# Kernel optimization log

Measured on AMD Instinct MI355X. Metric: run time of the kernel, lower is better.

## Reference

```python
import jax, jax.numpy as jnp
import numpy as np

B, N = 2048, 8192
K = 64          # subset size / number of relaxation steps
TAU = 1.0
EPS = 1e-10


def setup_inputs() -> dict:
    key = jax.random.key(0)
    k1, k2 = jax.random.split(key)
    scores = jax.random.normal(k1, (B, N), dtype=jnp.float32)
    # Gumbel(0,1) noise, same as torch.distributions.Gumbel(zeros, ones).sample()
    u = jax.random.uniform(k2, (B, N), dtype=jnp.float32, minval=1e-20, maxval=1.0)
    g = -jnp.log(-jnp.log(u))
    return {"scores": scores, "g": g}


def reference(scores, g):
    # Perturb scores with Gumbel noise
    s0 = scores + g  # [B, N]
    khot0 = jnp.zeros_like(s0)
    onehot0 = jnp.zeros_like(s0)

    def step(carry, _):
        s, khot, onehot_approx = carry
        khot_mask = jnp.maximum(1.0 - onehot_approx, EPS)   # suppress picked items
        s = s + jnp.log(khot_mask)
        onehot_approx = jax.nn.softmax(s / TAU, axis=1)
        return (s, khot + onehot_approx, onehot_approx), None

    (_, khot, _), _ = jax.lax.scan(step, (s0, khot0, onehot0), None, length=K)
    # hard=False -> return relaxed k-hot vector
    return khot
```

## Files before the change

kernel.cpp:

```cpp
#include <hip/hip_runtime.h>
#include <math.h>


#define BROWS 2048
#define NCOLS 8192
#define KSTEPS 64

#define THREADS 256
#define EPT (NCOLS / THREADS)

__global__ __launch_bounds__(THREADS, 4) void gumbel_subset_kernel(
    const float* __restrict__ scores,
    const float* __restrict__ g,
    float* __restrict__ out)
{
    const int row = blockIdx.x;
    const int t = threadIdx.x;
    const float* __restrict__ srow = scores + (size_t)row * NCOLS;
    const float* __restrict__ grow = g + (size_t)row * NCOLS;
    float* __restrict__ orow = out + (size_t)row * NCOLS;

    float v[EPT];
    float kh[EPT];

    float m = -INFINITY;
#pragma unroll
    for (int c = 0; c < EPT / 4; ++c) {
        const int idx = c * (THREADS * 4) + t * 4;
        const float4 a = *reinterpret_cast<const float4*>(srow + idx);
        const float4 b = *reinterpret_cast<const float4*>(grow + idx);
        const float s0 = a.x + b.x;
        const float s1 = a.y + b.y;
        const float s2 = a.z + b.z;
        const float s3 = a.w + b.w;
        v[c * 4 + 0] = s0;
        v[c * 4 + 1] = s1;
        v[c * 4 + 2] = s2;
        v[c * 4 + 3] = s3;
        m = fmaxf(m, fmaxf(fmaxf(s0, s1), fmaxf(s2, s3)));
    }

    __shared__ float red[2][8];
    const int wave = t >> 6;
    const int lane = t & 63;

#pragma unroll
    for (int off = 32; off > 0; off >>= 1)
        m = fmaxf(m, __shfl_xor(m, off, 64));
    if (lane == 0) red[0][wave] = m;
    __syncthreads();
    m = fmaxf(fmaxf(red[0][0], red[0][1]), fmaxf(red[0][2], red[0][3]));
    __syncthreads();

#pragma unroll
    for (int e = 0; e < EPT; ++e) {
        v[e] = __expf(v[e] - m);
        kh[e] = 0.0f;
    }

#pragma unroll 2
    for (int it = 0; it < KSTEPS; ++it) {
        float s = 0.0f;
#pragma unroll
        for (int e = 0; e < EPT; ++e) s += v[e];
#pragma unroll
        for (int off = 32; off > 0; off >>= 1)
            s += __shfl_xor(s, off, 64);

        const int buf = it & 1;
        if (lane == 0) red[buf][wave] = s;
        __syncthreads();
        const float S = (red[buf][0] + red[buf][1]) + (red[buf][2] + red[buf][3]);
        const float rinv = __builtin_amdgcn_rcpf(S);

#pragma unroll
        for (int e = 0; e < EPT; ++e) {
            const float w = v[e] * rinv;
            kh[e] += w;
            v[e] = __builtin_fmaf(-w, v[e], v[e]);
        }
    }

#pragma unroll
    for (int c = 0; c < EPT / 4; ++c) {
        const int idx = c * (THREADS * 4) + t * 4;
        float4 o;
        o.x = kh[c * 4 + 0];
        o.y = kh[c * 4 + 1];
        o.z = kh[c * 4 + 2];
        o.w = kh[c * 4 + 3];
        *reinterpret_cast<float4*>(orow + idx) = o;
    }
}

extern "C" void kernel_launch(void* const* d_in, const int* in_sizes, int n_in,
                              void* d_out, int out_size, void* d_ws, size_t ws_size,
                              hipStream_t stream) {
    const float* scores = (const float*)d_in[0];
    const float* g = (const float*)d_in[1];
    float* out = (float*)d_out;
    (void)in_sizes; (void)n_in; (void)out_size; (void)d_ws; (void)ws_size;

    gumbel_subset_kernel<<<BROWS, THREADS, 0, stream>>>(scores, g, out);
}
```

Before: 110.6 us.

## Double threads per row and fuse row-sum into the update loop

```diff
diff --git a/kernel.cpp b/kernel.cpp
--- a/kernel.cpp
+++ b/kernel.cpp
@@ -6,10 +6,11 @@
 #define NCOLS 8192
 #define KSTEPS 64
 
-#define THREADS 256
+#define THREADS 512
 #define EPT (NCOLS / THREADS)
+#define NWAVE (THREADS / 64)
 
-__global__ __launch_bounds__(THREADS, 4) void gumbel_subset_kernel(
+__global__ __launch_bounds__(THREADS, 8) void gumbel_subset_kernel(
     const float* __restrict__ scores,
     const float* __restrict__ g,
     float* __restrict__ out)
@@ -40,7 +41,7 @@
         m = fmaxf(m, fmaxf(fmaxf(s0, s1), fmaxf(s2, s3)));
     }
 
-    __shared__ float red[2][8];
+    __shared__ float red[2][NWAVE];
     const int wave = t >> 6;
     const int lane = t & 63;
 
@@ -49,20 +50,24 @@
         m = fmaxf(m, __shfl_xor(m, off, 64));
     if (lane == 0) red[0][wave] = m;
     __syncthreads();
-    m = fmaxf(fmaxf(red[0][0], red[0][1]), fmaxf(red[0][2], red[0][3]));
+    m = fmaxf(fmaxf(fmaxf(red[0][0], red[0][1]), fmaxf(red[0][2], red[0][3])),
+              fmaxf(fmaxf(red[0][4], red[0][5]), fmaxf(red[0][6], red[0][7])));
     __syncthreads();
 
+    float sa = 0.0f, sb = 0.0f, sc = 0.0f, sd = 0.0f;
 #pragma unroll
-    for (int e = 0; e < EPT; ++e) {
-        v[e] = __expf(v[e] - m);
-        kh[e] = 0.0f;
+    for (int e = 0; e < EPT; e += 4) {
+        v[e + 0] = __expf(v[e + 0] - m);
+        v[e + 1] = __expf(v[e + 1] - m);
+        v[e + 2] = __expf(v[e + 2] - m);
+        v[e + 3] = __expf(v[e + 3] - m);
+        kh[e + 0] = 0.0f; kh[e + 1] = 0.0f; kh[e + 2] = 0.0f; kh[e + 3] = 0.0f;
+        sa += v[e + 0]; sb += v[e + 1]; sc += v[e + 2]; sd += v[e + 3];
     }
 
 #pragma unroll 2
     for (int it = 0; it < KSTEPS; ++it) {
-        float s = 0.0f;
-#pragma unroll
-        for (int e = 0; e < EPT; ++e) s += v[e];
+        float s = (sa + sb) + (sc + sd);
 #pragma unroll
         for (int off = 32; off > 0; off >>= 1)
             s += __shfl_xor(s, off, 64);
@@ -70,14 +75,23 @@
         const int buf = it & 1;
         if (lane == 0) red[buf][wave] = s;
         __syncthreads();
-        const float S = (red[buf][0] + red[buf][1]) + (red[buf][2] + red[buf][3]);
+        const float S = ((red[buf][0] + red[buf][1]) + (red[buf][2] + red[buf][3])) +
+                        ((red[buf][4] + red[buf][5]) + (red[buf][6] + red[buf][7]));
         const float rinv = __builtin_amdgcn_rcpf(S);
 
+        sa = 0.0f; sb = 0.0f; sc = 0.0f; sd = 0.0f;
 #pragma unroll
-        for (int e = 0; e < EPT; ++e) {
-            const float w = v[e] * rinv;
-            kh[e] += w;
-            v[e] = __builtin_fmaf(-w, v[e], v[e]);
+        for (int e = 0; e < EPT; e += 4) {
+            const float w0 = v[e + 0] * rinv;
+            const float w1 = v[e + 1] * rinv;
+            const float w2 = v[e + 2] * rinv;
+            const float w3 = v[e + 3] * rinv;
+            kh[e + 0] += w0; kh[e + 1] += w1; kh[e + 2] += w2; kh[e + 3] += w3;
+            v[e + 0] = __builtin_fmaf(-w0, v[e + 0], v[e + 0]);
+            v[e + 1] = __builtin_fmaf(-w1, v[e + 1], v[e + 1]);
+            v[e + 2] = __builtin_fmaf(-w2, v[e + 2], v[e + 2]);
+            v[e + 3] = __builtin_fmaf(-w3, v[e + 3], v[e + 3]);
+            sa += v[e + 0]; sb += v[e + 1]; sc += v[e + 2]; sd += v[e + 3];
         }
     }
 
```

Result: slower. 130.4 us (+17.9%).

## Store softmax state in packed fp16 and fuse row-sum into the update pass

Applied to the files above, without the earlier changes.

```diff
diff --git a/kernel.cpp b/kernel.cpp
--- a/kernel.cpp
+++ b/kernel.cpp
@@ -1,6 +1,8 @@
 #include <hip/hip_runtime.h>
 #include <math.h>
 
+
+typedef _Float16 h2 __attribute__((ext_vector_type(2)));
 
 #define BROWS 2048
 #define NCOLS 8192
@@ -8,6 +10,8 @@
 
 #define THREADS 256
 #define EPT (NCOLS / THREADS)
+#define NPAIR (EPT / 2)
+#define NWAVE (THREADS / 64)
 
 __global__ __launch_bounds__(THREADS, 4) void gumbel_subset_kernel(
     const float* __restrict__ scores,
@@ -20,27 +24,22 @@
     const float* __restrict__ grow = g + (size_t)row * NCOLS;
     float* __restrict__ orow = out + (size_t)row * NCOLS;
 
-    float v[EPT];
-    float kh[EPT];
-
+    float s0[EPT];
     float m = -INFINITY;
 #pragma unroll
     for (int c = 0; c < EPT / 4; ++c) {
         const int idx = c * (THREADS * 4) + t * 4;
         const float4 a = *reinterpret_cast<const float4*>(srow + idx);
         const float4 b = *reinterpret_cast<const float4*>(grow + idx);
-        const float s0 = a.x + b.x;
-        const float s1 = a.y + b.y;
-        const float s2 = a.z + b.z;
-        const float s3 = a.w + b.w;
-        v[c * 4 + 0] = s0;
-        v[c * 4 + 1] = s1;
-        v[c * 4 + 2] = s2;
-        v[c * 4 + 3] = s3;
-        m = fmaxf(m, fmaxf(fmaxf(s0, s1), fmaxf(s2, s3)));
+        s0[c * 4 + 0] = a.x + b.x;
+        s0[c * 4 + 1] = a.y + b.y;
+        s0[c * 4 + 2] = a.z + b.z;
+        s0[c * 4 + 3] = a.w + b.w;
+        m = fmaxf(m, fmaxf(fmaxf(s0[c * 4 + 0], s0[c * 4 + 1]),
+                           fmaxf(s0[c * 4 + 2], s0[c * 4 + 3])));
     }
 
-    __shared__ float red[2][8];
+    __shared__ float red[2][NWAVE];
     const int wave = t >> 6;
     const int lane = t & 63;
 
@@ -52,17 +51,21 @@
     m = fmaxf(fmaxf(red[0][0], red[0][1]), fmaxf(red[0][2], red[0][3]));
     __syncthreads();
 
+    h2 v[NPAIR];
+    h2 kh[NPAIR];
+    float part = 0.0f;
 #pragma unroll
-    for (int e = 0; e < EPT; ++e) {
-        v[e] = __expf(v[e] - m);
-        kh[e] = 0.0f;
+    for (int p = 0; p < NPAIR; ++p) {
+        const float e0 = __expf(s0[2 * p + 0] - m);
+        const float e1 = __expf(s0[2 * p + 1] - m);
+        v[p] = (h2){(_Float16)e0, (_Float16)e1};
+        kh[p] = (h2){(_Float16)0.0f, (_Float16)0.0f};
+        part += e0 + e1;
     }
 
 #pragma unroll 2
     for (int it = 0; it < KSTEPS; ++it) {
-        float s = 0.0f;
-#pragma unroll
-        for (int e = 0; e < EPT; ++e) s += v[e];
+        float s = part;
 #pragma unroll
         for (int off = 32; off > 0; off >>= 1)
             s += __shfl_xor(s, off, 64);
@@ -71,24 +74,39 @@
         if (lane == 0) red[buf][wave] = s;
         __syncthreads();
         const float S = (red[buf][0] + red[buf][1]) + (red[buf][2] + red[buf][3]);
-        const float rinv = __builtin_amdgcn_rcpf(S);
+        const float rinvf = __builtin_amdgcn_rcpf(S);
+        const _Float16 rh = (_Float16)rinvf;
+        const h2 rinv2 = (h2){rh, rh};
 
+        h2 a0 = (h2){(_Float16)0.0f, (_Float16)0.0f};
+        h2 a1 = a0, a2 = a0, a3 = a0;
 #pragma unroll
-        for (int e = 0; e < EPT; ++e) {
-            const float w = v[e] * rinv;
-            kh[e] += w;
-            v[e] = __builtin_fmaf(-w, v[e], v[e]);
+        for (int p = 0; p < NPAIR; p += 4) {
+            const h2 w0 = v[p + 0] * rinv2;
+            const h2 w1 = v[p + 1] * rinv2;
+            const h2 w2 = v[p + 2] * rinv2;
+            const h2 w3 = v[p + 3] * rinv2;
+            kh[p + 0] += w0; kh[p + 1] += w1; kh[p + 2] += w2; kh[p + 3] += w3;
+            v[p + 0] = __builtin_elementwise_fma(-w0, v[p + 0], v[p + 0]);
+            v[p + 1] = __builtin_elementwise_fma(-w1, v[p + 1], v[p + 1]);
+            v[p + 2] = __builtin_elementwise_fma(-w2, v[p + 2], v[p + 2]);
+            v[p + 3] = __builtin_elementwise_fma(-w3, v[p + 3], v[p + 3]);
+            a0 += v[p + 0]; a1 += v[p + 1]; a2 += v[p + 2]; a3 += v[p + 3];
         }
+        const h2 a01 = a0 + a1;
+        const h2 a23 = a2 + a3;
+        const h2 aa = a01 + a23;
+        part = (float)aa.x + (float)aa.y;
     }
 
 #pragma unroll
     for (int c = 0; c < EPT / 4; ++c) {
         const int idx = c * (THREADS * 4) + t * 4;
         float4 o;
-        o.x = kh[c * 4 + 0];
-        o.y = kh[c * 4 + 1];
-        o.z = kh[c * 4 + 2];
-        o.w = kh[c * 4 + 3];
+        o.x = (float)kh[2 * c + 0].x;
+        o.y = (float)kh[2 * c + 0].y;
+        o.z = (float)kh[2 * c + 1].x;
+        o.w = (float)kh[2 * c + 1].y;
         *reinterpret_cast<float4*>(orow + idx) = o;
     }
 }
```

New measurement: 103.8 us. 6.1% less time.

## Pack softmax state in fp16 pairs, process two rows per block, fuse sum

Applied to the files above, without the earlier changes.

```diff
diff --git a/kernel.cpp b/kernel.cpp
--- a/kernel.cpp
+++ b/kernel.cpp
@@ -1,95 +1,141 @@
 #include <hip/hip_runtime.h>
 #include <math.h>
 
+
+typedef _Float16 h2 __attribute__((ext_vector_type(2)));
 
 #define BROWS 2048
 #define NCOLS 8192
 #define KSTEPS 64
 
 #define THREADS 256
+#define RPB 2
 #define EPT (NCOLS / THREADS)
+#define NPAIR (EPT / 2)
+#define NWAVE (THREADS / 64)
 
-__global__ __launch_bounds__(THREADS, 4) void gumbel_subset_kernel(
+__global__ __launch_bounds__(THREADS, 2) void gumbel_subset_kernel(
     const float* __restrict__ scores,
     const float* __restrict__ g,
     float* __restrict__ out)
 {
-    const int row = blockIdx.x;
     const int t = threadIdx.x;
-    const float* __restrict__ srow = scores + (size_t)row * NCOLS;
-    const float* __restrict__ grow = g + (size_t)row * NCOLS;
-    float* __restrict__ orow = out + (size_t)row * NCOLS;
+    const size_t baseA = (size_t)(blockIdx.x * RPB) * NCOLS;
+    const size_t baseB = baseA + NCOLS;
 
-    float v[EPT];
-    float kh[EPT];
-
-    float m = -INFINITY;
+    float sA[EPT], sB[EPT];
+    float mA = -INFINITY, mB = -INFINITY;
 #pragma unroll
     for (int c = 0; c < EPT / 4; ++c) {
         const int idx = c * (THREADS * 4) + t * 4;
-        const float4 a = *reinterpret_cast<const float4*>(srow + idx);
-        const float4 b = *reinterpret_cast<const float4*>(grow + idx);
-        const float s0 = a.x + b.x;
-        const float s1 = a.y + b.y;
-        const float s2 = a.z + b.z;
-        const float s3 = a.w + b.w;
-        v[c * 4 + 0] = s0;
-        v[c * 4 + 1] = s1;
-        v[c * 4 + 2] = s2;
-        v[c * 4 + 3] = s3;
-        m = fmaxf(m, fmaxf(fmaxf(s0, s1), fmaxf(s2, s3)));
+        const float4 a0 = *reinterpret_cast<const float4*>(scores + baseA + idx);
+        const float4 g0 = *reinterpret_cast<const float4*>(g + baseA + idx);
+        sA[c * 4 + 0] = a0.x + g0.x;
+        sA[c * 4 + 1] = a0.y + g0.y;
+        sA[c * 4 + 2] = a0.z + g0.z;
+        sA[c * 4 + 3] = a0.w + g0.w;
+        mA = fmaxf(mA, fmaxf(fmaxf(sA[c * 4 + 0], sA[c * 4 + 1]),
+                             fmaxf(sA[c * 4 + 2], sA[c * 4 + 3])));
+        const float4 a1 = *reinterpret_cast<const float4*>(scores + baseB + idx);
+        const float4 g1 = *reinterpret_cast<const float4*>(g + baseB + idx);
+        sB[c * 4 + 0] = a1.x + g1.x;
+        sB[c * 4 + 1] = a1.y + g1.y;
+        sB[c * 4 + 2] = a1.z + g1.z;
+        sB[c * 4 + 3] = a1.w + g1.w;
+        mB = fmaxf(mB, fmaxf(fmaxf(sB[c * 4 + 0], sB[c * 4 + 1]),
+                             fmaxf(sB[c * 4 + 2], sB[c * 4 + 3])));
     }
 
-    __shared__ float red[2][8];
+    __shared__ float red[2][2 * NWAVE];
     const int wave = t >> 6;
     const int lane = t & 63;
 
 #pragma unroll
-    for (int off = 32; off > 0; off >>= 1)
-        m = fmaxf(m, __shfl_xor(m, off, 64));
-    if (lane == 0) red[0][wave] = m;
+    for (int off = 32; off > 0; off >>= 1) {
+        mA = fmaxf(mA, __shfl_xor(mA, off, 64));
+        mB = fmaxf(mB, __shfl_xor(mB, off, 64));
+    }
+    if (lane == 0) { red[0][wave] = mA; red[0][NWAVE + wave] = mB; }
     __syncthreads();
-    m = fmaxf(fmaxf(red[0][0], red[0][1]), fmaxf(red[0][2], red[0][3]));
+    mA = fmaxf(fmaxf(red[0][0], red[0][1]), fmaxf(red[0][2], red[0][3]));
+    mB = fmaxf(fmaxf(red[0][4], red[0][5]), fmaxf(red[0][6], red[0][7]));
     __syncthreads();
 
+    h2 vA[NPAIR], khA[NPAIR], vB[NPAIR], khB[NPAIR];
+    float partA = 0.0f, partB = 0.0f;
 #pragma unroll
-    for (int e = 0; e < EPT; ++e) {
-        v[e] = __expf(v[e] - m);
-        kh[e] = 0.0f;
+    for (int p = 0; p < NPAIR; ++p) {
+        const float eA0 = __expf(sA[2 * p + 0] - mA);
+        const float eA1 = __expf(sA[2 * p + 1] - mA);
+        vA[p] = (h2){(_Float16)eA0, (_Float16)eA1};
+        khA[p] = (h2){(_Float16)0.0f, (_Float16)0.0f};
+        partA += eA0 + eA1;
+        const float eB0 = __expf(sB[2 * p + 0] - mB);
+        const float eB1 = __expf(sB[2 * p + 1] - mB);
+        vB[p] = (h2){(_Float16)eB0, (_Float16)eB1};
+        khB[p] = (h2){(_Float16)0.0f, (_Float16)0.0f};
+        partB += eB0 + eB1;
     }
 
 #pragma unroll 2
     for (int it = 0; it < KSTEPS; ++it) {
-        float s = 0.0f;
+        float sa = partA, sb = partB;
 #pragma unroll
-        for (int e = 0; e < EPT; ++e) s += v[e];
-#pragma unroll
-        for (int off = 32; off > 0; off >>= 1)
-            s += __shfl_xor(s, off, 64);
+        for (int off = 32; off > 0; off >>= 1) {
+            sa += __shfl_xor(sa, off, 64);
+            sb += __shfl_xor(sb, off, 64);
+        }
 
         const int buf = it & 1;
-        if (lane == 0) red[buf][wave] = s;
+        if (lane == 0) { red[buf][wave] = sa; red[buf][NWAVE + wave] = sb; }
         __syncthreads();
-        const float S = (red[buf][0] + red[buf][1]) + (red[buf][2] + red[buf][3]);
-        const float rinv = __builtin_amdgcn_rcpf(S);
+        const float SA = (red[buf][0] + red[buf][1]) + (red[buf][2] + red[buf][3]);
+        const float SB = (red[buf][4] + red[buf][5]) + (red[buf][6] + red[buf][7]);
+        const float rAf = __builtin_amdgcn_rcpf(SA);
+        const float rBf = __builtin_amdgcn_rcpf(SB);
+        const _Float16 rAh = (_Float16)rAf;
+        const _Float16 rBh = (_Float16)rBf;
+        const h2 rA2 = (h2){rAh, rAh};
+        const h2 rB2 = (h2){rBh, rBh};
 
+        h2 z = (h2){(_Float16)0.0f, (_Float16)0.0f};
+        h2 aA0 = z, aA1 = z, aB0 = z, aB1 = z;
 #pragma unroll
-        for (int e = 0; e < EPT; ++e) {
-            const float w = v[e] * rinv;
-            kh[e] += w;
-            v[e] = __builtin_fmaf(-w, v[e], v[e]);
+        for (int p = 0; p < NPAIR; p += 2) {
+            const h2 wA0 = vA[p + 0] * rA2;
+            const h2 wA1 = vA[p + 1] * rA2;
+            const h2 wB0 = vB[p + 0] * rB2;
+            const h2 wB1 = vB[p + 1] * rB2;
+            khA[p + 0] += wA0; khA[p + 1] += wA1;
+            khB[p + 0] += wB0; khB[p + 1] += wB1;
+            vA[p + 0] = __builtin_elementwise_fma(-wA0, vA[p + 0], vA[p + 0]);
+            vA[p + 1] = __builtin_elementwise_fma(-wA1, vA[p + 1], vA[p + 1]);
+            vB[p + 0] = __builtin_elementwise_fma(-wB0, vB[p + 0], vB[p + 0]);
+            vB[p + 1] = __builtin_elementwise_fma(-wB1, vB[p + 1], vB[p + 1]);
+            aA0 += vA[p + 0]; aA1 += vA[p + 1];
+            aB0 += vB[p + 0]; aB1 += vB[p + 1];
         }
+        const h2 aa = aA0 + aA1;
+        const h2 bb = aB0 + aB1;
+        partA = (float)aa.x + (float)aa.y;
+        partB = (float)bb.x + (float)bb.y;
     }
 
 #pragma unroll
     for (int c = 0; c < EPT / 4; ++c) {
         const int idx = c * (THREADS * 4) + t * 4;
-        float4 o;
-        o.x = kh[c * 4 + 0];
-        o.y = kh[c * 4 + 1];
-        o.z = kh[c * 4 + 2];
-        o.w = kh[c * 4 + 3];
-        *reinterpret_cast<float4*>(orow + idx) = o;
+        float4 oA;
+        oA.x = (float)khA[2 * c + 0].x;
+        oA.y = (float)khA[2 * c + 0].y;
+        oA.z = (float)khA[2 * c + 1].x;
+        oA.w = (float)khA[2 * c + 1].y;
+        *reinterpret_cast<float4*>(out + baseA + idx) = oA;
+        float4 oB;
+        oB.x = (float)khB[2 * c + 0].x;
+        oB.y = (float)khB[2 * c + 0].y;
+        oB.z = (float)khB[2 * c + 1].x;
+        oB.w = (float)khB[2 * c + 1].y;
+        *reinterpret_cast<float4*>(out + baseB + idx) = oB;
     }
 }
 
@@ -101,5 +147,5 @@
     float* out = (float*)d_out;
     (void)in_sizes; (void)n_in; (void)out_size; (void)d_ws; (void)ws_size;
 
-    gumbel_subset_kernel<<<BROWS, THREADS, 0, stream>>>(scores, g, out);
+    gumbel_subset_kernel<<<BROWS / RPB, THREADS, 0, stream>>>(scores, g, out);
 }
```

After: 115.8 us. +4.6%, slower.
